# Performance work log

Hardware: AMD Instinct MI355X
Metric: run time of the kernel (lower is better)

## Reference

```python
import jax, jax.numpy as jnp
import numpy as np

N = 50000          # nodes
E = 800000         # edges
H, C = 8, 32       # heads, channels per head
HC = H * C         # 256
IN = 4             # input feature dim
SLOPE = 0.2        # LeakyReLU negative slope (PyG default)
EPS = 1e-16        # PyG softmax denominator eps


def gat_layer(x, src, dst, ea, W, a_s, a_d, W_e, a_e, b, add_self_loops):
    """Single PyG-style GATConv with edge_dim=1. x:[N,in], ea:[E,1]."""
    if add_self_loops:
        # fill_value='mean': self-loop edge_attr = mean of incoming edge_attr per node
        ones = jnp.ones((src.shape[0], 1), ea.dtype)
        cnt = jax.ops.segment_sum(ones, dst, num_segments=N)
        loop_ea = jax.ops.segment_sum(ea, dst, num_segments=N) / jnp.maximum(cnt, 1.0)
        loop = jnp.arange(N, dtype=src.dtype)
        src = jnp.concatenate([src, loop])
        dst = jnp.concatenate([dst, loop])
        ea = jnp.concatenate([ea, loop_ea], axis=0)
    h = (x @ W).reshape(-1, H, C)                       # [N,H,C] shared src/dst proj
    al_s = jnp.einsum('nhc,hc->nh', h, a_s)              # [N,H]
    al_d = jnp.einsum('nhc,hc->nh', h, a_d)              # [N,H]
    # lin_edge is [1 -> H*C] with no bias, so (lin_edge(ea) * att_edge).sum(-1)
    # collapses to ea * w_e with w_e[h] = sum_c W_e[h,c]*a_e[h,c]
    w_e = jnp.sum(W_e * a_e, axis=-1)                    # [H]
    logits = al_s[src] + al_d[dst] + ea * w_e[None, :]   # [E,H]
    logits = jax.nn.leaky_relu(logits, SLOPE)
    # segment softmax over destination node
    m = jax.ops.segment_max(logits, dst, num_segments=N)
    m = jnp.where(jnp.isfinite(m), m, 0.0)
    p = jnp.exp(logits - m[dst])
    denom = jax.ops.segment_sum(p, dst, num_segments=N)
    alpha = p / (denom[dst] + EPS)                       # [E,H]
    out = jax.ops.segment_sum(h[src] * alpha[:, :, None], dst, num_segments=N)
    return out.reshape(-1, HC) + b                       # concat heads + bias


def setup_inputs() -> dict:
    key = jax.random.key(0)
    ks = jax.random.split(key, 24)
    inp = {
        'x': jax.random.normal(ks[0], (N, IN), jnp.float32),
        'edge_index': jax.random.randint(ks[1], (2, E), 0, N, jnp.int32),
        'edge_attr': jax.random.uniform(ks[2], (E, 1), jnp.float32),
    }
    in_dims = [IN, HC, HC]
    ki = 3
    for l in range(3):
        d = in_dims[l]
        inp[f'W{l+1}'] = jax.random.normal(ks[ki], (d, HC), jnp.float32) * (1.0 / np.sqrt(d)); ki += 1
        inp[f'as{l+1}'] = jax.random.normal(ks[ki], (H, C), jnp.float32) * 0.1; ki += 1
        inp[f'ad{l+1}'] = jax.random.normal(ks[ki], (H, C), jnp.float32) * 0.1; ki += 1
        inp[f'We{l+1}'] = jax.random.normal(ks[ki], (H, C), jnp.float32) * 0.1; ki += 1
        inp[f'ae{l+1}'] = jax.random.normal(ks[ki], (H, C), jnp.float32) * 0.1; ki += 1
        inp[f'b{l+1}'] = jnp.zeros((HC,), jnp.float32)
    return inp


def reference(x, edge_index, edge_attr,
              W1, as1, ad1, We1, ae1, b1,
              W2, as2, ad2, We2, ae2, b2,
              W3, as3, ad3, We3, ae3, b3):
    src, dst = edge_index[0], edge_index[1]
    h = jax.nn.relu(gat_layer(x, src, dst, edge_attr, W1, as1, ad1, We1, ae1, b1, False))
    h = jax.nn.relu(gat_layer(h, src, dst, edge_attr, W2, as2, ad2, We2, ae2, b2, True))
    h = jax.nn.relu(gat_layer(h, src, dst, edge_attr, W3, as3, ad3, We3, ae3, b3, True))
    return h
```

## Files before the change

### kernel.cpp

```cpp
#include <hip/hip_runtime.h>
#include <hip/hip_fp16.h>
#include <math.h>

#define HEADS 8
#define HC 256
#define SLOPE 0.2f
#define SM_EPS 1e-16f
#define LDA 40

typedef __attribute__((ext_vector_type(4))) _Float16 half4v;
typedef __attribute__((ext_vector_type(8))) _Float16 half8;
typedef __attribute__((ext_vector_type(4))) float f32x4;

__global__ void hist_kernel(const int* __restrict__ dst, int* __restrict__ cnt,
                            int* __restrict__ rank, int E) {
  int e = blockIdx.x * blockDim.x + threadIdx.x;
  if (e < E) rank[e] = atomicAdd(&cnt[dst[e]], 1);
}

__global__ void scan_blocks(const int* __restrict__ cnt, int* __restrict__ excl,
                            int* __restrict__ bsums, int N) {
  __shared__ int wsum[16];
  int t = threadIdx.x;
  int i = blockIdx.x * 1024 + t;
  int v = (i < N) ? cnt[i] : 0;
  int lane = t & 63, w = t >> 6;
  int s = v;
  #pragma unroll
  for (int off = 1; off < 64; off <<= 1) {
    int u = __shfl_up(s, off);
    if (lane >= off) s += u;
  }
  if (lane == 63) wsum[w] = s;
  __syncthreads();
  if (w == 0) {
    int ws = (lane < 16) ? wsum[lane] : 0;
    #pragma unroll
    for (int off = 1; off < 16; off <<= 1) {
      int u = __shfl_up(ws, off);
      if (lane >= off) ws += u;
    }
    if (lane < 16) wsum[lane] = ws;
  }
  __syncthreads();
  int wo = (w == 0) ? 0 : wsum[w - 1];
  int incl = s + wo;
  if (i < N) excl[i] = incl - v;
  if (t == 1023) bsums[blockIdx.x] = incl;
}

__global__ void scan_sums(int* __restrict__ bsums, int nb) {
  int lane = threadIdx.x;
  int carry = 0;
  for (int c0 = 0; c0 < nb; c0 += 64) {
    int idx = c0 + lane;
    int v = (idx < nb) ? bsums[idx] : 0;
    int s = v;
    #pragma unroll
    for (int off = 1; off < 64; off <<= 1) {
      int u = __shfl_up(s, off);
      if (lane >= off) s += u;
    }
    if (idx < nb) bsums[idx] = carry + s - v;
    carry += __shfl(s, 63);
  }
}

__global__ void scan_apply(const int* __restrict__ bsums, int* __restrict__ row_ptr,
                           int N, int E) {
  int i = blockIdx.x * blockDim.x + threadIdx.x;
  if (i < N) row_ptr[i] += bsums[i >> 10];
  if (i == 0) row_ptr[N] = E;
}

__global__ void fill_kernel(const int* __restrict__ src, const int* __restrict__ dst,
                            const float* __restrict__ ea, const int* __restrict__ row_ptr,
                            const int* __restrict__ rank, int2* __restrict__ srcea, int E) {
  int e = blockIdx.x * blockDim.x + threadIdx.x;
  if (e < E) {
    int pos = row_ptr[dst[e]] + rank[e];
    srcea[pos] = make_int2(src[e], __float_as_int(ea[e]));
  }
}

__global__ void wek_all(const float* __restrict__ We1, const float* __restrict__ ae1,
                        const float* __restrict__ We2, const float* __restrict__ ae2,
                        const float* __restrict__ We3, const float* __restrict__ ae3,
                        float* __restrict__ wev) {
  int l = blockIdx.x;
  int t = threadIdx.x;
  const float* We = (l == 0) ? We1 : (l == 1) ? We2 : We3;
  const float* ae = (l == 0) ? ae1 : (l == 1) ? ae2 : ae3;
  float p = 0.f;
  #pragma unroll
  for (int i = 0; i < 4; i++) p += We[t * 4 + i] * ae[t * 4 + i];
  p += __shfl_xor(p, 1);
  p += __shfl_xor(p, 2);
  p += __shfl_xor(p, 4);
  if ((t & 7) == 0) wev[l * 8 + (t >> 3)] = p;
}

__global__ void wsplit_kernel(const float* __restrict__ W, __half* __restrict__ WT) {
  int k = blockIdx.x;
  int n = threadIdx.x;
  WT[n * HC + k] = (__half)W[k * HC + n];
}

__global__ void l1_prep(const float* __restrict__ x, const float* __restrict__ W,
                        const float* __restrict__ a_s, const float* __restrict__ a_d,
                        float* __restrict__ als, float* __restrict__ ald, int M) {
  __shared__ float4 Xs[16];
  int t = threadIdx.x;
  int m0 = blockIdx.x * 16;
  if (t < 16 && (m0 + t) < M) Xs[t] = *(const float4*)(x + (size_t)(m0 + t) * 4);
  __syncthreads();
  float w0 = W[0 * HC + t], w1 = W[1 * HC + t], w2 = W[2 * HC + t], w3 = W[3 * HC + t];
  float as_ = a_s[t], ad_ = a_d[t];
  #pragma unroll
  for (int r = 0; r < 16; r++) {
    int m = m0 + r;
    if (m < M) {
      float4 a = Xs[r];
      float h = a.x * w0 + a.y * w1 + a.z * w2 + a.w * w3;
      float ps = h * as_;
      float pd = h * ad_;
      #pragma unroll
      for (int mm = 1; mm < 32; mm <<= 1) {
        ps += __shfl_xor(ps, mm);
        pd += __shfl_xor(pd, mm);
      }
      if ((t & 31) == 0) {
        als[(size_t)m * HEADS + (t >> 5)] = ps;
        ald[(size_t)m * HEADS + (t >> 5)] = pd;
      }
    }
  }
}

__global__ __launch_bounds__(256) void mfma_gemm(
    const __half* __restrict__ A, const __half* __restrict__ WT,
    const float* __restrict__ a_s, const float* __restrict__ a_d,
    __half* __restrict__ Hh, float* __restrict__ als, float* __restrict__ ald, int M) {
  __shared__ _Float16 sA[64 * LDA], sB[128 * LDA];
  int t = threadIdx.x;
  int bm = blockIdx.x >> 1, bn = blockIdx.x & 1;
  int m0 = bm * 64, n0 = bn * 128;
  int wave = t >> 6, lane = t & 63, quad = lane >> 4, l16 = lane & 15;
  int sr = t >> 2;
  int sk = (t & 3) * 8;

  f32x4 acc[8];
  #pragma unroll
  for (int c = 0; c < 8; c++) acc[c] = (f32x4){0.f, 0.f, 0.f, 0.f};

  size_t ar = (size_t)min(m0 + sr, M - 1) * HC;
  size_t br0 = (size_t)(n0 + sr) * HC;
  size_t br1 = (size_t)(n0 + sr + 64) * HC;

  half8 pA = *(const half8*)(A + ar + sk);
  half8 pB0 = *(const half8*)(WT + br0 + sk);
  half8 pB1 = *(const half8*)(WT + br1 + sk);

  for (int k0 = 0; k0 < HC; k0 += 32) {
    __syncthreads();
    *(half8*)(sA + sr * LDA + sk) = pA;
    *(half8*)(sB + sr * LDA + sk) = pB0;
    *(half8*)(sB + (sr + 64) * LDA + sk) = pB1;
    __syncthreads();
    int kn = k0 + 32;
    if (kn < HC) {
      pA = *(const half8*)(A + ar + kn + sk);
      pB0 = *(const half8*)(WT + br0 + kn + sk);
      pB1 = *(const half8*)(WT + br1 + kn + sk);
    }
    half8 av = *(const half8*)(sA + (wave * 16 + l16) * LDA + quad * 8);
    #pragma unroll
    for (int c = 0; c < 8; c++) {
      half8 bv = *(const half8*)(sB + (c * 16 + l16) * LDA + quad * 8);
      acc[c] = __builtin_amdgcn_mfma_f32_16x16x32_f16(av, bv, acc[c], 0, 0, 0);
    }
  }

  float asv[8], adv[8];
  #pragma unroll
  for (int c = 0; c < 8; c++) {
    int col = n0 + c * 16 + l16;
    asv[c] = a_s[col];
    adv[c] = a_d[col];
  }
  #pragma unroll
  for (int reg = 0; reg < 4; reg++) {
    int m = m0 + wave * 16 + quad * 4 + reg;
    bool ok = (m < M);
    if (ok) {
      #pragma unroll
      for (int c = 0; c < 8; c++)
        Hh[(size_t)m * HC + n0 + c * 16 + l16] = (__half)acc[c][reg];
    }
    #pragma unroll
    for (int d = 0; d < 4; d++) {
      float ps = acc[2 * d][reg] * asv[2 * d] + acc[2 * d + 1][reg] * asv[2 * d + 1];
      float pd = acc[2 * d][reg] * adv[2 * d] + acc[2 * d + 1][reg] * adv[2 * d + 1];
      #pragma unroll
      for (int mm = 1; mm < 16; mm <<= 1) {
        ps += __shfl_xor(ps, mm);
        pd += __shfl_xor(pd, mm);
      }
      if (ok && l16 == 0) {
        als[(size_t)m * HEADS + (n0 >> 5) + d] = ps;
        ald[(size_t)m * HEADS + (n0 >> 5) + d] = pd;
      }
    }
  }
}

__global__ __launch_bounds__(256) void accum_l1_kernel(
    const int2* __restrict__ srcea, const int* __restrict__ row_ptr,
    const float* __restrict__ x, const float* __restrict__ W,
    const float* __restrict__ als, const float* __restrict__ ald,
    const float* __restrict__ wev, const float* __restrict__ bias,
    __half* __restrict__ Ah, int N) {
  int n = blockIdx.x * 4 + (threadIdx.x >> 6);
  if (n >= N) return;
  int lane = threadIdx.x & 63;
  int h_t = lane >> 3;
  int cbase = lane * 4;
  int base = row_ptr[n], deg = row_ptr[n + 1] - base;
  int ubase = __builtin_amdgcn_readfirstlane(base);
  int udeg = __builtin_amdgcn_readfirstlane(deg);
  float ald_h = ald[(size_t)n * HEADS + h_t];
  float we_h = wev[h_t];
  float4 wr0 = *(const float4*)(W + 0 * HC + cbase);
  float4 wr1 = *(const float4*)(W + 1 * HC + cbase);
  float4 wr2 = *(const float4*)(W + 2 * HC + cbase);
  float4 wr3 = *(const float4*)(W + 3 * HC + cbase);

  float den = 0.f;
  float4 acc = make_float4(0.f, 0.f, 0.f, 0.f);
  #pragma unroll 8
  for (int j = 0; j < udeg; j++) {
    int2 se = srcea[ubase + j];
    int s = __builtin_amdgcn_readfirstlane(se.x);
    float eav = __int_as_float(se.y);
    float l = als[(size_t)s * HEADS + h_t] + ald_h + eav * we_h;
    l = (l > 0.f) ? l : SLOPE * l;
    float p = __expf(l);
    den += p;
    float4 xv = *(const float4*)(x + (size_t)s * 4);
    float h0 = xv.x * wr0.x + xv.y * wr1.x + xv.z * wr2.x + xv.w * wr3.x;
    float h1 = xv.x * wr0.y + xv.y * wr1.y + xv.z * wr2.y + xv.w * wr3.y;
    float h2 = xv.x * wr0.z + xv.y * wr1.z + xv.z * wr2.z + xv.w * wr3.z;
    float h3 = xv.x * wr0.w + xv.y * wr1.w + xv.z * wr2.w + xv.w * wr3.w;
    acc.x = fmaf(p, h0, acc.x);
    acc.y = fmaf(p, h1, acc.y);
    acc.z = fmaf(p, h2, acc.z);
    acc.w = fmaf(p, h3, acc.w);
  }

  float rinv = 1.0f / (den + SM_EPS);
  float4 o;
  o.x = fmaxf(fmaf(acc.x, rinv, bias[cbase + 0]), 0.f);
  o.y = fmaxf(fmaf(acc.y, rinv, bias[cbase + 1]), 0.f);
  o.z = fmaxf(fmaf(acc.z, rinv, bias[cbase + 2]), 0.f);
  o.w = fmaxf(fmaf(acc.w, rinv, bias[cbase + 3]), 0.f);
  half4v hv;
  hv.x = (_Float16)o.x;
  hv.y = (_Float16)o.y;
  hv.z = (_Float16)o.z;
  hv.w = (_Float16)o.w;
  *(half4v*)(Ah + (size_t)n * HC + cbase) = hv;
}

template <int SPLIT>
__global__ __launch_bounds__(256) void accum_kernel(
    const int2* __restrict__ srcea, const int* __restrict__ row_ptr,
    const __half* __restrict__ h, const float* __restrict__ als,
    const float* __restrict__ ald, const float* __restrict__ wev,
    const float* __restrict__ bias, float* __restrict__ out,
    __half* __restrict__ Ah, int N) {
  int n = blockIdx.x * 4 + (threadIdx.x >> 6);
  if (n >= N) return;
  int lane = threadIdx.x & 63;
  int h_t = lane >> 3;
  int base = row_ptr[n], deg = row_ptr[n + 1] - base;
  int ubase = __builtin_amdgcn_readfirstlane(base);
  int udeg = __builtin_amdgcn_readfirstlane(deg);
  float ald_h = ald[(size_t)n * HEADS + h_t];
  float we_h = wev[h_t];

  float den = 0.f, easum = 0.f;
  float4 acc = make_float4(0.f, 0.f, 0.f, 0.f);
  #pragma unroll 8
  for (int j = 0; j < udeg; j++) {
    int2 se = srcea[ubase + j];
    int s = se.x;
    float eav = __int_as_float(se.y);
    easum += eav;
    float l = als[(size_t)s * HEADS + h_t] + ald_h + eav * we_h;
    l = (l > 0.f) ? l : SLOPE * l;
    float p = __expf(l);
    den += p;
    const half4v hv = *(const half4v*)(h + (size_t)s * HC + lane * 4);
    acc.x = fmaf(p, (float)hv.x, acc.x);
    acc.y = fmaf(p, (float)hv.y, acc.y);
    acc.z = fmaf(p, (float)hv.z, acc.z);
    acc.w = fmaf(p, (float)hv.w, acc.w);
  }
  {
    float mean_ea = easum / fmaxf((float)udeg, 1.0f);
    float l = als[(size_t)n * HEADS + h_t] + ald_h + mean_ea * we_h;
    l = (l > 0.f) ? l : SLOPE * l;
    float p = __expf(l);
    den += p;
    const half4v hv = *(const half4v*)(h + (size_t)n * HC + lane * 4);
    acc.x = fmaf(p, (float)hv.x, acc.x);
    acc.y = fmaf(p, (float)hv.y, acc.y);
    acc.z = fmaf(p, (float)hv.z, acc.z);
    acc.w = fmaf(p, (float)hv.w, acc.w);
  }

  float rinv = 1.0f / (den + SM_EPS);
  int cbase = lane * 4;
  float4 o;
  o.x = fmaxf(fmaf(acc.x, rinv, bias[cbase + 0]), 0.f);
  o.y = fmaxf(fmaf(acc.y, rinv, bias[cbase + 1]), 0.f);
  o.z = fmaxf(fmaf(acc.z, rinv, bias[cbase + 2]), 0.f);
  o.w = fmaxf(fmaf(acc.w, rinv, bias[cbase + 3]), 0.f);
  if (SPLIT) {
    half4v hv;
    hv.x = (_Float16)o.x;
    hv.y = (_Float16)o.y;
    hv.z = (_Float16)o.z;
    hv.w = (_Float16)o.w;
    *(half4v*)(Ah + (size_t)n * HC + cbase) = hv;
  } else {
    *(float4*)(out + (size_t)n * HC + cbase) = o;
  }
}

extern "C" void kernel_launch(void* const* d_in, const int* in_sizes, int n_in,
                              void* d_out, int out_size, void* d_ws, size_t ws_size,
                              hipStream_t stream) {
  const float* x = (const float*)d_in[0];
  const int* ei = (const int*)d_in[1];
  const float* ea = (const float*)d_in[2];
  int N = in_sizes[0] / 4;
  int E = in_sizes[1] / 2;
  const int* src = ei;
  const int* dst = ei + E;

  const float* W[3];
  const float* Asw[3];
  const float* Adw[3];
  const float* Wew[3];
  const float* Aew[3];
  const float* Bw[3];
  for (int l = 0; l < 3; l++) {
    W[l]   = (const float*)d_in[3 + 6 * l + 0];
    Asw[l] = (const float*)d_in[3 + 6 * l + 1];
    Adw[l] = (const float*)d_in[3 + 6 * l + 2];
    Wew[l] = (const float*)d_in[3 + 6 * l + 3];
    Aew[l] = (const float*)d_in[3 + 6 * l + 4];
    Bw[l]  = (const float*)d_in[3 + 6 * l + 5];
  }

  char* w = (char*)d_ws;
  auto alloc = [&](size_t bytes) {
    char* p = w;
    w += (bytes + 255) & ~(size_t)255;
    return p;
  };
  __half* Hh    = (__half*)alloc((size_t)N * HC * 2);
  __half* Ah    = (__half*)alloc((size_t)N * HC * 2);
  int2* srcea   = (int2*)alloc((size_t)E * 8);
  int* rank     = (int*)alloc((size_t)E * 4);
  __half* WT2   = (__half*)alloc((size_t)HC * HC * 2);
  __half* WT3   = (__half*)alloc((size_t)HC * HC * 2);
  float* als    = (float*)alloc((size_t)N * HEADS * 4);
  float* ald    = (float*)alloc((size_t)N * HEADS * 4);
  float* wev    = (float*)alloc(24 * 4);
  int* cnt      = (int*)alloc((size_t)N * 4);
  int* row_ptr  = (int*)alloc(((size_t)N + 1) * 4);
  int* bsums    = (int*)alloc(((size_t)N / 1024 + 2) * 4);
  float* outf = (float*)d_out;

  int nb = (N + 1023) / 1024;
  (void)hipMemsetAsync(cnt, 0, (size_t)N * 4, stream);
  hist_kernel<<<(E + 255) / 256, 256, 0, stream>>>(dst, cnt, rank, E);
  scan_blocks<<<nb, 1024, 0, stream>>>(cnt, row_ptr, bsums, N);
  scan_sums<<<1, 64, 0, stream>>>(bsums, nb);
  scan_apply<<<(N + 255) / 256, 256, 0, stream>>>(bsums, row_ptr, N, E);
  fill_kernel<<<(E + 255) / 256, 256, 0, stream>>>(src, dst, ea, row_ptr, rank,
                                                   srcea, E);
  wek_all<<<3, 64, 0, stream>>>(Wew[0], Aew[0], Wew[1], Aew[1], Wew[2], Aew[2], wev);
  wsplit_kernel<<<HC, HC, 0, stream>>>(W[1], WT2);
  wsplit_kernel<<<HC, HC, 0, stream>>>(W[2], WT3);

  int agg_grid = (N + 3) / 4;
  int gemm_grid = ((N + 63) / 64) * 2;

  l1_prep<<<(N + 15) / 16, 256, 0, stream>>>(x, W[0], Asw[0], Adw[0], als, ald, N);
  accum_l1_kernel<<<agg_grid, 256, 0, stream>>>(srcea, row_ptr, x, W[0], als, ald,
                                                wev + 0, Bw[0], Ah, N);

  mfma_gemm<<<gemm_grid, 256, 0, stream>>>(Ah, WT2, Asw[1], Adw[1], Hh, als, ald, N);
  accum_kernel<1><<<agg_grid, 256, 0, stream>>>(srcea, row_ptr, Hh, als, ald,
                                                wev + 8, Bw[1], nullptr, Ah, N);

  mfma_gemm<<<gemm_grid, 256, 0, stream>>>(Ah, WT3, Asw[2], Adw[2], Hh, als, ald, N);
  accum_kernel<0><<<agg_grid, 256, 0, stream>>>(srcea, row_ptr, Hh, als, ald,
                                                wev + 16, Bw[2], outf, nullptr, N);
}
```

Before: 446.3 us.

## Enlarge GEMM M-tile to 128 rows and merge small prep kernels

The MFMA GEMM now computes a 128x128 output tile per block, with each wave holding two 16-row sub-tiles so every B fragment loaded from shared memory feeds two MFMAs. This halves the B-tile traffic per output and halves the grid size. Separately, the weight transpose and edge-weight reduction kernels are merged into one launch to cut launch overhead. The larger tile doubles accumulator registers and shared memory per block, which may reduce occupancy, and the smaller grid (about 782 blocks) gives fewer blocks to spread across CUs.

Result: no change. 452.1 us (+1.3%).

```diff
diff --git a/kernel.cpp b/kernel.cpp
--- a/kernel.cpp
+++ b/kernel.cpp
@@ -83,27 +83,32 @@
   }
 }
 
-__global__ void wek_all(const float* __restrict__ We1, const float* __restrict__ ae1,
-                        const float* __restrict__ We2, const float* __restrict__ ae2,
-                        const float* __restrict__ We3, const float* __restrict__ ae3,
-                        float* __restrict__ wev) {
-  int l = blockIdx.x;
+__global__ void prep_kernel(const float* __restrict__ W2, __half* __restrict__ WT2,
+                            const float* __restrict__ W3, __half* __restrict__ WT3,
+                            const float* __restrict__ We1, const float* __restrict__ ae1,
+                            const float* __restrict__ We2, const float* __restrict__ ae2,
+                            const float* __restrict__ We3, const float* __restrict__ ae3,
+                            float* __restrict__ wev) {
+  int b = blockIdx.x;
   int t = threadIdx.x;
-  const float* We = (l == 0) ? We1 : (l == 1) ? We2 : We3;
-  const float* ae = (l == 0) ? ae1 : (l == 1) ? ae2 : ae3;
-  float p = 0.f;
-  #pragma unroll
-  for (int i = 0; i < 4; i++) p += We[t * 4 + i] * ae[t * 4 + i];
-  p += __shfl_xor(p, 1);
-  p += __shfl_xor(p, 2);
-  p += __shfl_xor(p, 4);
-  if ((t & 7) == 0) wev[l * 8 + (t >> 3)] = p;
-}
-
-__global__ void wsplit_kernel(const float* __restrict__ W, __half* __restrict__ WT) {
-  int k = blockIdx.x;
-  int n = threadIdx.x;
-  WT[n * HC + k] = (__half)W[k * HC + n];
+  if (b < 256) {
+    WT2[t * HC + b] = (__half)W2[b * HC + t];
+  } else if (b < 512) {
+    int k = b - 256;
+    WT3[t * HC + k] = (__half)W3[k * HC + t];
+  } else {
+    if (t >= 64) return;
+    int l = b - 512;
+    const float* We = (l == 0) ? We1 : (l == 1) ? We2 : We3;
+    const float* ae = (l == 0) ? ae1 : (l == 1) ? ae2 : ae3;
+    float p = 0.f;
+    #pragma unroll
+    for (int i = 0; i < 4; i++) p += We[t * 4 + i] * ae[t * 4 + i];
+    p += __shfl_xor(p, 1);
+    p += __shfl_xor(p, 2);
+    p += __shfl_xor(p, 4);
+    if ((t & 7) == 0) wev[l * 8 + (t >> 3)] = p;
+  }
 }
 
 __global__ void l1_prep(const float* __restrict__ x, const float* __restrict__ W,
@@ -141,43 +146,54 @@
     const __half* __restrict__ A, const __half* __restrict__ WT,
     const float* __restrict__ a_s, const float* __restrict__ a_d,
     __half* __restrict__ Hh, float* __restrict__ als, float* __restrict__ ald, int M) {
-  __shared__ _Float16 sA[64 * LDA], sB[128 * LDA];
+  __shared__ _Float16 sA[128 * LDA], sB[128 * LDA];
   int t = threadIdx.x;
   int bm = blockIdx.x >> 1, bn = blockIdx.x & 1;
-  int m0 = bm * 64, n0 = bn * 128;
+  int m0 = bm * 128, n0 = bn * 128;
   int wave = t >> 6, lane = t & 63, quad = lane >> 4, l16 = lane & 15;
   int sr = t >> 2;
   int sk = (t & 3) * 8;
 
-  f32x4 acc[8];
+  f32x4 acc[2][8];
   #pragma unroll
-  for (int c = 0; c < 8; c++) acc[c] = (f32x4){0.f, 0.f, 0.f, 0.f};
-
-  size_t ar = (size_t)min(m0 + sr, M - 1) * HC;
+  for (int s = 0; s < 2; s++)
+    #pragma unroll
+    for (int c = 0; c < 8; c++) acc[s][c] = (f32x4){0.f, 0.f, 0.f, 0.f};
+
+  size_t ar0 = (size_t)min(m0 + sr, M - 1) * HC;
+  size_t ar1 = (size_t)min(m0 + sr + 64, M - 1) * HC;
   size_t br0 = (size_t)(n0 + sr) * HC;
   size_t br1 = (size_t)(n0 + sr + 64) * HC;
 
-  half8 pA = *(const half8*)(A + ar + sk);
+  half8 pA0 = *(const half8*)(A + ar0 + sk);
+  half8 pA1 = *(const half8*)(A + ar1 + sk);
   half8 pB0 = *(const half8*)(WT + br0 + sk);
   half8 pB1 = *(const half8*)(WT + br1 + sk);
 
   for (int k0 = 0; k0 < HC; k0 += 32) {
     __syncthreads();
-    *(half8*)(sA + sr * LDA + sk) = pA;
+    *(half8*)(sA + sr * LDA + sk) = pA0;
+    *(half8*)(sA + (sr + 64) * LDA + sk) = pA1;
     *(half8*)(sB + sr * LDA + sk) = pB0;
     *(half8*)(sB + (sr + 64) * LDA + sk) = pB1;
     __syncthreads();
     int kn = k0 + 32;
     if (kn < HC) {
-      pA = *(const half8*)(A + ar + kn + sk);
+      pA0 = *(const half8*)(A + ar0 + kn + sk);
+      pA1 = *(const half8*)(A + ar1 + kn + sk);
       pB0 = *(const half8*)(WT + br0 + kn + sk);
       pB1 = *(const half8*)(WT + br1 + kn + sk);
     }
-    half8 av = *(const half8*)(sA + (wave * 16 + l16) * LDA + quad * 8);
+    half8 av[2];
+    #pragma unroll
+    for (int s = 0; s < 2; s++)
+      av[s] = *(const half8*)(sA + (wave * 32 + s * 16 + l16) * LDA + quad * 8);
     #pragma unroll
     for (int c = 0; c < 8; c++) {
       half8 bv = *(const half8*)(sB + (c * 16 + l16) * LDA + quad * 8);
-      acc[c] = __builtin_amdgcn_mfma_f32_16x16x32_f16(av, bv, acc[c], 0, 0, 0);
+      #pragma unroll
+      for (int s = 0; s < 2; s++)
+        acc[s][c] = __builtin_amdgcn_mfma_f32_16x16x32_f16(av[s], bv, acc[s][c], 0, 0, 0);
     }
   }
 
@@ -189,26 +205,29 @@
     adv[c] = a_d[col];
   }
   #pragma unroll
-  for (int reg = 0; reg < 4; reg++) {
-    int m = m0 + wave * 16 + quad * 4 + reg;
-    bool ok = (m < M);
-    if (ok) {
+  for (int s = 0; s < 2; s++) {
+    #pragma unroll
+    for (int reg = 0; reg < 4; reg++) {
+      int m = m0 + wave * 32 + s * 16 + quad * 4 + reg;
+      bool ok = (m < M);
+      if (ok) {
+        #pragma unroll
+        for (int c = 0; c < 8; c++)
+          Hh[(size_t)m * HC + n0 + c * 16 + l16] = (__half)acc[s][c][reg];
+      }
       #pragma unroll
-      for (int c = 0; c < 8; c++)
-        Hh[(size_t)m * HC + n0 + c * 16 + l16] = (__half)acc[c][reg];
-    }
-    #pragma unroll
-    for (int d = 0; d < 4; d++) {
-      float ps = acc[2 * d][reg] * asv[2 * d] + acc[2 * d + 1][reg] * asv[2 * d + 1];
-      float pd = acc[2 * d][reg] * adv[2 * d] + acc[2 * d + 1][reg] * adv[2 * d + 1];
-      #pragma unroll
-      for (int mm = 1; mm < 16; mm <<= 1) {
-        ps += __shfl_xor(ps, mm);
-        pd += __shfl_xor(pd, mm);
-      }
-      if (ok && l16 == 0) {
-        als[(size_t)m * HEADS + (n0 >> 5) + d] = ps;
-        ald[(size_t)m * HEADS + (n0 >> 5) + d] = pd;
+      for (int d = 0; d < 4; d++) {
+        float ps = acc[s][2 * d][reg] * asv[2 * d] + acc[s][2 * d + 1][reg] * asv[2 * d + 1];
+        float pd = acc[s][2 * d][reg] * adv[2 * d] + acc[s][2 * d + 1][reg] * adv[2 * d + 1];
+        #pragma unroll
+        for (int mm = 1; mm < 16; mm <<= 1) {
+          ps += __shfl_xor(ps, mm);
+          pd += __shfl_xor(pd, mm);
+        }
+        if (ok && l16 == 0) {
+          als[(size_t)m * HEADS + (n0 >> 5) + d] = ps;
+          ald[(size_t)m * HEADS + (n0 >> 5) + d] = pd;
+        }
       }
     }
   }
@@ -392,12 +411,12 @@
   scan_apply<<<(N + 255) / 256, 256, 0, stream>>>(bsums, row_ptr, N, E);
   fill_kernel<<<(E + 255) / 256, 256, 0, stream>>>(src, dst, ea, row_ptr, rank,
                                                    srcea, E);
-  wek_all<<<3, 64, 0, stream>>>(Wew[0], Aew[0], Wew[1], Aew[1], Wew[2], Aew[2], wev);
-  wsplit_kernel<<<HC, HC, 0, stream>>>(W[1], WT2);
-  wsplit_kernel<<<HC, HC, 0, stream>>>(W[2], WT3);
+  prep_kernel<<<515, 256, 0, stream>>>(W[1], WT2, W[2], WT3,
+                                       Wew[0], Aew[0], Wew[1], Aew[1],
+                                       Wew[2], Aew[2], wev);
 
   int agg_grid = (N + 3) / 4;
-  int gemm_grid = ((N + 63) / 64) * 2;
+  int gemm_grid = ((N + 127) / 128) * 2;
 
   l1_prep<<<(N + 15) / 16, 256, 0, stream>>>(x, W[0], Asw[0], Adw[0], als, ald, N);
   accum_l1_kernel<<<agg_grid, 256, 0, stream>>>(srcea, row_ptr, x, W[0], als, ald,
```
